# Performance work log

Measured on AMD Instinct MI355X. Metric: run time of the kernel, lower is better.

Reference implementation:

```python
import jax, jax.numpy as jnp
import numpy as np

D = 128
L_SIZE = 65536
C_SIZE = 32768
E = 262144
N_ITERS = 4


def _mlp(x, w1, b1, w2, b2):
    # 2-layer satbench MLP: Linear -> relu -> Linear
    return jax.nn.relu(x @ w1 + b1) @ w2 + b2


def setup_inputs() -> dict:
    key = jax.random.key(0)
    ks = iter(jax.random.split(key, 32))

    def lin(fi, fo):
        # torch nn.Linear default init, stored as (in, out)
        bound = 1.0 / np.sqrt(fi)
        w = jax.random.uniform(next(ks), (fi, fo), minval=-bound, maxval=bound, dtype=jnp.float32)
        b = jax.random.uniform(next(ks), (fo,), minval=-bound, maxval=bound, dtype=jnp.float32)
        return w, b

    s = np.sqrt(2.0 / D).astype(np.float32)
    inp = {}
    inp['l_edge_index'] = jax.random.randint(next(ks), (E,), 0, L_SIZE, dtype=jnp.int64)
    inp['c_edge_index'] = jax.random.randint(next(ks), (E,), 0, C_SIZE, dtype=jnp.int64)
    inp['l_init'] = jax.random.normal(next(ks), (1, D), dtype=jnp.float32) * s
    inp['c_init'] = jax.random.normal(next(ks), (1, D), dtype=jnp.float32) * s
    inp['w_l2c1'], inp['b_l2c1'] = lin(D, D)
    inp['w_l2c2'], inp['b_l2c2'] = lin(D, D)
    inp['w_c2l1'], inp['b_c2l1'] = lin(D, D)
    inp['w_c2l2'], inp['b_c2l2'] = lin(D, D)
    inp['w_l2l1'], inp['b_l2l1'] = lin(D, D)
    inp['w_l2l2'], inp['b_l2l2'] = lin(D, D)
    inp['w_cu'], inp['b_cu'] = lin(2 * D, D)
    inp['w_lu'], inp['b_lu'] = lin(3 * D, D)
    inp['l_size'] = L_SIZE
    inp['c_size'] = C_SIZE
    return inp


def reference(l_edge_index, c_edge_index, l_init, c_init,
              w_l2c1, b_l2c1, w_l2c2, b_l2c2,
              w_c2l1, b_c2l1, w_c2l2, b_c2l2,
              w_l2l1, b_l2l1, w_l2l2, b_l2l2,
              w_cu, b_cu, w_lu, b_lu, l_size, c_size):
    d = l_init.shape[1]
    ones = jnp.ones((l_edge_index.shape[0], 1), dtype=l_init.dtype)
    l_deg = jax.ops.segment_sum(ones, l_edge_index, num_segments=l_size)   # (L,1)
    c_deg = jax.ops.segment_sum(ones, c_edge_index, num_segments=c_size)   # (C,1)
    degree_norm = jnp.sqrt(l_deg[l_edge_index]) * jnp.sqrt(c_deg[c_edge_index])  # (E,1)

    l_emb = jnp.tile(l_init, (l_size, 1))  # (L,d)
    c_emb = jnp.tile(c_init, (c_size, 1))  # (C,d)

    def step(carry, _):
        l_emb, c_emb = carry
        l2c_msg = _mlp(l_emb, w_l2c1, b_l2c1, w_l2c2, b_l2c2)[l_edge_index]  # (E,d)
        c2l_msg = _mlp(c_emb, w_c2l1, b_c2l1, w_c2l2, b_c2l2)[c_edge_index]  # (E,d)
        # swap positive/negative literal partner embeddings (pairs are adjacent rows)
        l2l_in = l_emb.reshape(l_size // 2, 2, d)[:, ::-1, :].reshape(l_size, d)
        l2l_msg = _mlp(l2l_in, w_l2l1, b_l2l1, w_l2l2, b_l2l2)              # (L,d)
        l2c_aggr = jax.ops.segment_sum(l2c_msg / degree_norm, c_edge_index, num_segments=c_size)
        c_new = jnp.concatenate([c_emb, l2c_aggr], axis=1) @ w_cu + b_cu
        c2l_aggr = jax.ops.segment_sum(c2l_msg / degree_norm, l_edge_index, num_segments=l_size)
        l_new = jnp.concatenate([l_emb, c2l_aggr, l2l_msg], axis=1) @ w_lu + b_lu
        return (l_new, c_new), None

    (l_emb, c_emb), _ = jax.lax.scan(step, (l_emb, c_emb), None, length=N_ITERS)
    return l_emb
```

## Files before the change

kernel.cpp:

```cpp
#include <hip/hip_runtime.h>
#include <hip/hip_bf16.h>

#define D_ 128
#define L_ 65536
#define C_ 32768
#define E_ 262144

typedef __hip_bfloat16 bf16;
typedef __attribute__((ext_vector_type(8))) short short8;
typedef __attribute__((ext_vector_type(4))) float f32x4;

__global__ void detect_k(const unsigned short* __restrict__ wmem,
                         const int* __restrict__ li, int* __restrict__ flags) {
    int t = blockIdx.x * 512 + threadIdx.x;
    if (t < 8192) {
        unsigned short h = wmem[2 * t];
        float v = __bfloat162float(*(const bf16*)&h);
        if (!(fabsf(v) < 0.5f)) atomicOr(&flags[0], 1);
    }
    if (t < 2048) {
        if (li[2 * t + 1] != 0) atomicOr(&flags[1], 1);
    }
}

__device__ __forceinline__ void split2(float v, unsigned short& h, unsigned short& l) {
    bf16 bh = __float2bfloat16(v);
    float fh = __bfloat162float(bh);
    bf16 bl = __float2bfloat16(v - fh);
    h = *(unsigned short*)&bh;
    l = *(unsigned short*)&bl;
}

__device__ __forceinline__ float ldf(const void* s, int i, int isf32) {
    return isf32 ? ((const float*)s)[i] : __bfloat162float(((const bf16*)s)[i]);
}

__global__ void fixdeg_k(const int* __restrict__ ls, const int* __restrict__ cs,
                         int* __restrict__ ld_idx, int* __restrict__ cd_idx,
                         int* __restrict__ ldeg, int* __restrict__ cdeg,
                         const int* __restrict__ flags) {
    int i = blockIdx.x * 256 + threadIdx.x;
    int is32 = flags[1];
    if (i < E_) {
        int v = is32 ? ls[i] : ls[2 * i];
        v = min(max(v, 0), L_ - 1);
        ld_idx[i] = v;
        atomicAdd(&ldeg[v], 1);
    } else {
        int j = i - E_;
        int v = is32 ? cs[j] : cs[2 * j];
        v = min(max(v, 0), C_ - 1);
        cd_idx[j] = v;
        atomicAdd(&cdeg[v], 1);
    }
}

__global__ void cvtwb_k(const void* s0, const void* s1, const void* s2, const void* s3,
                        const void* s4, const void* s5, const void* s6, const void* s7,
                        const void* t0, const void* t1, const void* t2, const void* t3,
                        const void* t4, const void* t5, const void* t6, const void* t7,
                        unsigned short* __restrict__ hi, unsigned short* __restrict__ lo,
                        float* __restrict__ bb, const int* __restrict__ flags) {
    int i = blockIdx.x * 256 + threadIdx.x;
    int isf = flags[0];
    if (i >= 180224) {
        int j = i - 180224;
        const void* src;
        switch (j >> 7) {
            case 0: src = t0; break; case 1: src = t1; break;
            case 2: src = t2; break; case 3: src = t3; break;
            case 4: src = t4; break; case 5: src = t5; break;
            case 6: src = t6; break; default: src = t7; break;
        }
        bb[j] = ldf(src, j & 127, isf);
        return;
    }
    const void* src; int K, base;
    if      (i <  16384) { src = s0; K = 128; base = 0; }
    else if (i <  32768) { src = s1; K = 128; base = 16384; }
    else if (i <  49152) { src = s2; K = 128; base = 32768; }
    else if (i <  65536) { src = s3; K = 128; base = 49152; }
    else if (i <  81920) { src = s4; K = 128; base = 65536; }
    else if (i <  98304) { src = s5; K = 128; base = 81920; }
    else if (i < 131072) { src = s6; K = 256; base = 98304; }
    else                 { src = s7; K = 384; base = 131072; }
    int e = i - base;
    int k = e >> 7, n = e & 127;
    float v = ldf(src, e, isf);
    unsigned short h, l;
    split2(v, h, l);
    hi[base + n * K + k] = h;
    lo[base + n * K + k] = l;
}

__global__ void init2_k(const void* __restrict__ lv, const void* __restrict__ cv,
                        float* __restrict__ lemb, float* __restrict__ cemb,
                        const int* __restrict__ flags) {
    int i4 = blockIdx.x * 256 + threadIdx.x;
    int isf = flags[0];
    const void* src; float* dst; int o;
    if (i4 < L_ * 32) { src = lv; dst = lemb; o = i4; }
    else              { src = cv; dst = cemb; o = i4 - L_ * 32; }
    int j = (o & 31) * 4;
    float4 v;
    v.x = ldf(src, j + 0, isf);
    v.y = ldf(src, j + 1, isf);
    v.z = ldf(src, j + 2, isf);
    v.w = ldf(src, j + 3, isf);
    ((float4*)dst)[o] = v;
}

__global__ void scan1b_k(const int* __restrict__ ldeg, const int* __restrict__ cdeg,
                         int* __restrict__ lout, int* __restrict__ cout,
                         int* __restrict__ bsumL, int* __restrict__ bsumC) {
    __shared__ int s[256];
    const int* in; int* out; int* bs; int tile;
    if (blockIdx.x < 256) { in = ldeg; out = lout; bs = bsumL; tile = blockIdx.x; }
    else                  { in = cdeg; out = cout; bs = bsumC; tile = blockIdx.x - 256; }
    int i = tile * 256 + threadIdx.x;
    int v = in[i];
    s[threadIdx.x] = v;
    __syncthreads();
#pragma unroll
    for (int off = 1; off < 256; off <<= 1) {
        int t = (threadIdx.x >= off) ? s[threadIdx.x - off] : 0;
        __syncthreads();
        s[threadIdx.x] += t;
        __syncthreads();
    }
    out[i] = s[threadIdx.x] - v;
    if (threadIdx.x == 255) bs[tile] = s[255];
}

__global__ void scan2b_k(int* __restrict__ bL, int* __restrict__ bC) {
    __shared__ int s[256];
    int* b = blockIdx.x ? bC : bL;
    int nb = blockIdx.x ? 128 : 256;
    int v = (threadIdx.x < nb) ? b[threadIdx.x] : 0;
    s[threadIdx.x] = v;
    __syncthreads();
#pragma unroll
    for (int off = 1; off < 256; off <<= 1) {
        int t = (threadIdx.x >= off) ? s[threadIdx.x - off] : 0;
        __syncthreads();
        s[threadIdx.x] += t;
        __syncthreads();
    }
    if (threadIdx.x < nb) b[threadIdx.x] = s[threadIdx.x] - v;
}

__global__ void scan3b_k(int* __restrict__ lptr, int* __restrict__ cptr,
                         const int* __restrict__ bsumL, const int* __restrict__ bsumC,
                         int* __restrict__ lcur, int* __restrict__ ccur,
                         const int* __restrict__ ldeg, const int* __restrict__ cdeg,
                         float* __restrict__ invsq_l, float* __restrict__ invsq_c) {
    int b = blockIdx.x, t = threadIdx.x;
    if (b < 256) {
        int i = b * 256 + t;
        int v = lptr[i] + bsumL[b];
        lptr[i] = v; lcur[i] = v;
        int d = ldeg[i];
        invsq_l[i] = d ? rsqrtf((float)d) : 0.0f;
    } else {
        int i = (b - 256) * 256 + t;
        int v = cptr[i] + bsumC[b - 256];
        cptr[i] = v; ccur[i] = v;
        int d = cdeg[i];
        invsq_c[i] = d ? rsqrtf((float)d) : 0.0f;
    }
}

__global__ void place_k(const int* __restrict__ li, const int* __restrict__ ci,
                        int* __restrict__ lcur, int* __restrict__ ccur,
                        int* __restrict__ l_other, int* __restrict__ c_other) {
    int e = blockIdx.x * 256 + threadIdx.x;
    if (e >= E_) return;
    int l = li[e], c = ci[e];
    int p = atomicAdd(&ccur[c], 1);
    c_other[p] = l;
    int q = atomicAdd(&lcur[l], 1);
    l_other[q] = c;
}

__global__ __launch_bounds__(256) void gather2_k(
    const int* __restrict__ cptr, const int* __restrict__ cdeg, const int* __restrict__ c_other,
    const unsigned int* __restrict__ lmsg, const float* __restrict__ invsq_c, float* __restrict__ caggr,
    const int* __restrict__ lptr, const int* __restrict__ ldeg, const int* __restrict__ l_other,
    const unsigned int* __restrict__ cmsg, const float* __restrict__ invsq_l, float* __restrict__ laggr,
    int nC) {
    int node = (blockIdx.x * 256 + threadIdx.x) >> 6;
    int lane = threadIdx.x & 63;
    bool cside = node < nC;
    int j = cside ? node : node - nC;
    const int* ptr = cside ? cptr : lptr;
    const int* dg  = cside ? cdeg : ldeg;
    const int* oth = cside ? c_other : l_other;
    const unsigned int* msg = cside ? lmsg : cmsg;
    float sc = (cside ? invsq_c : invsq_l)[j];
    float* out = cside ? caggr : laggr;
    int s = ptr[j], cnt = dg[j];
    float2 a0 = {0.f, 0.f}, a1 = {0.f, 0.f};
    int k = 0;
    for (; k + 4 <= cnt; k += 4) {
        int o0 = oth[s + k], o1 = oth[s + k + 1], o2 = oth[s + k + 2], o3 = oth[s + k + 3];
        unsigned int u0 = msg[(size_t)o0 * 64 + lane];
        unsigned int u1 = msg[(size_t)o1 * 64 + lane];
        unsigned int u2 = msg[(size_t)o2 * 64 + lane];
        unsigned int u3 = msg[(size_t)o3 * 64 + lane];
        a0.x += __uint_as_float(u0 << 16) + __uint_as_float(u2 << 16);
        a0.y += __uint_as_float(u0 & 0xffff0000u) + __uint_as_float(u2 & 0xffff0000u);
        a1.x += __uint_as_float(u1 << 16) + __uint_as_float(u3 << 16);
        a1.y += __uint_as_float(u1 & 0xffff0000u) + __uint_as_float(u3 & 0xffff0000u);
    }
    for (; k < cnt; k++) {
        int o = oth[s + k];
        unsigned int u = msg[(size_t)o * 64 + lane];
        a0.x += __uint_as_float(u << 16);
        a0.y += __uint_as_float(u & 0xffff0000u);
    }
    a0.x = (a0.x + a1.x) * sc;
    a0.y = (a0.y + a1.y) * sc;
    *(float2*)&out[(size_t)j * D_ + 2 * lane] = a0;
}

__global__ __launch_bounds__(512, 4) void mlp3_k(
    const float* __restrict__ l_cur, const float* __restrict__ c_cur,
    const unsigned short* __restrict__ wt_hi, const unsigned short* __restrict__ wt_lo,
    const float* __restrict__ bb,
    const float* __restrict__ invsq_l, const float* __restrict__ invsq_c,
    bf16* __restrict__ l_msg, bf16* __restrict__ c_msg, bf16* __restrict__ l2lb,
    int nL, int nC) {
    __shared__ char smem[66048];
    unsigned short (*a_hi)[40] = (unsigned short(*)[40])(smem);
    unsigned short (*a_lo)[40] = (unsigned short(*)[40])(smem + 10240);
    unsigned short* h_hi = (unsigned short*)(smem);
    unsigned short* h_lo = (unsigned short*)(smem + 32768);
    float* scv = (float*)(smem + 65536);

    int b = blockIdx.x, seg, tile;
    if (b < nL)           { seg = 0; tile = b; }
    else if (b < nL + nC) { seg = 1; tile = b - nL; }
    else                  { seg = 2; tile = b - nL - nC; }
    const float* A = (seg == 1) ? c_cur : l_cur;
    bf16* outp = (seg == 0) ? l_msg : (seg == 1) ? c_msg : l2lb;
    const float* invsq = (seg == 0) ? invsq_l : (seg == 1) ? invsq_c : nullptr;
    const unsigned short* W1h = wt_hi + seg * 32768;
    const unsigned short* W1l = wt_lo + seg * 32768;
    const unsigned short* W2h = W1h + 16384;
    const unsigned short* W2l = W1l + 16384;
    const float* b1v = bb + seg * 256;
    const float* b2v = b1v + 128;
    const int swap = (seg == 2);

    const int t = threadIdx.x;
    const int br0 = tile * 128;
    const int w = t >> 6, lane = t & 63;
    const int wr = w >> 2, wc = w & 3;
    const int quad = lane >> 4, cl = lane & 15;

    if (t < 128) scv[t] = invsq ? invsq[br0 + t] : 1.0f;

    f32x4 acc[4][2];
#pragma unroll
    for (int i = 0; i < 4; i++)
#pragma unroll
        for (int j = 0; j < 2; j++) acc[i][j] = (f32x4){0.f, 0.f, 0.f, 0.f};

    for (int kt = 0; kt < 128; kt += 32) {
#pragma unroll
        for (int i = 0; i < 2; i++) {
            int f = t + 512 * i;
            int r = f >> 3, kq = f & 7;
            int gr = br0 + r;
            if (swap) gr ^= 1;
            const float4 v = *(const float4*)&A[(size_t)gr * D_ + kt + 4 * kq];
            unsigned short h0, l0, h1, l1, h2, l2, h3, l3;
            split2(v.x, h0, l0); split2(v.y, h1, l1);
            split2(v.z, h2, l2); split2(v.w, h3, l3);
            *(ushort4*)&a_hi[r][4 * kq] = make_ushort4(h0, h1, h2, h3);
            *(ushort4*)&a_lo[r][4 * kq] = make_ushort4(l0, l1, l2, l3);
        }
        __syncthreads();
        short8 af_h[4], af_l[4];
#pragma unroll
        for (int i = 0; i < 4; i++) {
            int row = 64 * wr + 16 * i + cl;
            af_h[i] = *(const short8*)&a_hi[row][quad * 8];
            af_l[i] = *(const short8*)&a_lo[row][quad * 8];
        }
#pragma unroll
        for (int j = 0; j < 2; j++) {
            int col = 32 * wc + 16 * j + cl;
            short8 bf_h = *(const short8*)&W1h[(size_t)col * 128 + kt + quad * 8];
            short8 bf_l = *(const short8*)&W1l[(size_t)col * 128 + kt + quad * 8];
#pragma unroll
            for (int i = 0; i < 4; i++) {
                acc[i][j] = __builtin_amdgcn_mfma_f32_16x16x32_bf16(af_h[i], bf_h, acc[i][j], 0, 0, 0);
                acc[i][j] = __builtin_amdgcn_mfma_f32_16x16x32_bf16(af_h[i], bf_l, acc[i][j], 0, 0, 0);
                acc[i][j] = __builtin_amdgcn_mfma_f32_16x16x32_bf16(af_l[i], bf_h, acc[i][j], 0, 0, 0);
            }
        }
        __syncthreads();
    }
#pragma unroll
    for (int j = 0; j < 2; j++) {
        int col = 32 * wc + 16 * j + cl;
        float bv = b1v[col];
        int g = col >> 3, go = col & 7;
#pragma unroll
        for (int i = 0; i < 4; i++) {
            int rloc = 64 * wr + 16 * i + quad * 4;
#pragma unroll
            for (int rg = 0; rg < 4; rg++) {
                float v = fmaxf(acc[i][j][rg] + bv, 0.0f);
                unsigned short hh, ll;
                split2(v, hh, ll);
                int r = rloc + rg;
                int off = r * 128 + ((g ^ (r & 15)) << 3) + go;
                h_hi[off] = hh;
                h_lo[off] = ll;
            }
        }
    }
    __syncthreads();
#pragma unroll
    for (int i = 0; i < 4; i++)
#pragma unroll
        for (int j = 0; j < 2; j++) acc[i][j] = (f32x4){0.f, 0.f, 0.f, 0.f};

    for (int kt = 0; kt < 128; kt += 32) {
        short8 af_h[4], af_l[4];
        int gbase = (kt >> 3) + quad;
#pragma unroll
        for (int i = 0; i < 4; i++) {
            int r = 64 * wr + 16 * i + cl;
            int off = r * 128 + ((gbase ^ cl) << 3);
            af_h[i] = *(const short8*)&h_hi[off];
            af_l[i] = *(const short8*)&h_lo[off];
        }
#pragma unroll
        for (int j = 0; j < 2; j++) {
            int col = 32 * wc + 16 * j + cl;
            const short8 bf_h = *(const short8*)&W2h[(size_t)col * 128 + kt + quad * 8];
            const short8 bf_l = *(const short8*)&W2l[(size_t)col * 128 + kt + quad * 8];
#pragma unroll
            for (int i = 0; i < 4; i++) {
                acc[i][j] = __builtin_amdgcn_mfma_f32_16x16x32_bf16(af_h[i], bf_h, acc[i][j], 0, 0, 0);
                acc[i][j] = __builtin_amdgcn_mfma_f32_16x16x32_bf16(af_h[i], bf_l, acc[i][j], 0, 0, 0);
                acc[i][j] = __builtin_amdgcn_mfma_f32_16x16x32_bf16(af_l[i], bf_h, acc[i][j], 0, 0, 0);
            }
        }
    }
#pragma unroll
    for (int j = 0; j < 2; j++) {
        int col = 32 * wc + 16 * j + cl;
        float bv = b2v[col];
#pragma unroll
        for (int i = 0; i < 4; i++) {
            int rloc = 64 * wr + 16 * i + quad * 4;
#pragma unroll
            for (int rg = 0; rg < 4; rg++)
                outp[(size_t)(br0 + rloc + rg) * D_ + col] =
                    __float2bfloat16((acc[i][j][rg] + bv) * scv[rloc + rg]);
        }
    }
}

template <int FINAL>
__global__ __launch_bounds__(256, 2) void update_k(
    const float* __restrict__ l_cur, const float* __restrict__ c_cur,
    const float* __restrict__ laggr, const float* __restrict__ caggr,
    const bf16* __restrict__ l2lb,
    const unsigned short* __restrict__ wt_hi, const unsigned short* __restrict__ wt_lo,
    const float* __restrict__ bb,
    float* __restrict__ c_nxt, float* __restrict__ l_nxt,
    void* __restrict__ dout, const int* __restrict__ flags) {
    __shared__ unsigned short a_hi[128][40], a_lo[128][40];
    __shared__ unsigned short b_hi[128][40], b_lo[128][40];
    const int t = threadIdx.x;
    int b = blockIdx.x;
    const bool cseg = (!FINAL) && (b < 256);
    const int tile = (FINAL || cseg) ? b : b - 256;
    const int K = cseg ? 256 : 384;
    const float* A0 = cseg ? c_cur : l_cur;
    const float* A1 = cseg ? caggr : laggr;
    const unsigned short* Wh = wt_hi + (cseg ? 98304 : 131072);
    const unsigned short* Wl = wt_lo + (cseg ? 98304 : 131072);
    const float* bias = bb + (cseg ? 768 : 896);
    const int br0 = tile * 128;
    const int w = t >> 6, lane = t & 63;
    const int wr = w >> 1, wc = w & 1;
    const int quad = lane >> 4, cl = lane & 15;

    f32x4 acc[4][4];
#pragma unroll
    for (int i = 0; i < 4; i++)
#pragma unroll
        for (int j = 0; j < 4; j++) acc[i][j] = (f32x4){0.f, 0.f, 0.f, 0.f};

    for (int kt = 0; kt < K; kt += 32) {
        const bool haslo = (kt < 256);
        const int koff = kt & 127;
#pragma unroll
        for (int i = 0; i < 4; i++) {
            int f = t + 256 * i;
            int r = f >> 3, kq = f & 7;
            if (haslo) {
                const float* As = (kt < 128) ? A0 : A1;
                const float4 v = *(const float4*)&As[(size_t)(br0 + r) * D_ + koff + 4 * kq];
                unsigned short h0, l0, h1, l1, h2, l2, h3, l3;
                split2(v.x, h0, l0); split2(v.y, h1, l1);
                split2(v.z, h2, l2); split2(v.w, h3, l3);
                *(ushort4*)&a_hi[r][4 * kq] = make_ushort4(h0, h1, h2, h3);
                *(ushort4*)&a_lo[r][4 * kq] = make_ushort4(l0, l1, l2, l3);
            } else {
                *(ushort4*)&a_hi[r][4 * kq] =
                    *(const ushort4*)&l2lb[(size_t)(br0 + r) * D_ + koff + 4 * kq];
            }
            *(ushort4*)&b_hi[r][4 * kq] = *(const ushort4*)&Wh[(size_t)r * K + kt + 4 * kq];
            *(ushort4*)&b_lo[r][4 * kq] = *(const ushort4*)&Wl[(size_t)r * K + kt + 4 * kq];
        }
        __syncthreads();
        short8 af_h[4], af_l[4];
#pragma unroll
        for (int i = 0; i < 4; i++) {
            int row = 64 * wr + 16 * i + cl;
            af_h[i] = *(const short8*)&a_hi[row][quad * 8];
            if (haslo) af_l[i] = *(const short8*)&a_lo[row][quad * 8];
        }
#pragma unroll
        for (int j = 0; j < 4; j++) {
            int col = 64 * wc + 16 * j + cl;
            short8 bf_h = *(const short8*)&b_hi[col][quad * 8];
            short8 bf_l = *(const short8*)&b_lo[col][quad * 8];
#pragma unroll
            for (int i = 0; i < 4; i++) {
                acc[i][j] = __builtin_amdgcn_mfma_f32_16x16x32_bf16(af_h[i], bf_h, acc[i][j], 0, 0, 0);
                acc[i][j] = __builtin_amdgcn_mfma_f32_16x16x32_bf16(af_h[i], bf_l, acc[i][j], 0, 0, 0);
                if (haslo)
                    acc[i][j] = __builtin_amdgcn_mfma_f32_16x16x32_bf16(af_l[i], bf_h, acc[i][j], 0, 0, 0);
            }
        }
        __syncthreads();
    }
    const int f32out = FINAL ? flags[0] : 1;
#pragma unroll
    for (int j = 0; j < 4; j++) {
        int col = 64 * wc + 16 * j + cl;
        float bv = bias[col];
#pragma unroll
        for (int i = 0; i < 4; i++) {
            int rbase = br0 + 64 * wr + 16 * i + quad * 4;
#pragma unroll
            for (int rg = 0; rg < 4; rg++) {
                float v = acc[i][j][rg] + bv;
                size_t idx = (size_t)(rbase + rg) * D_ + col;
                if (FINAL) {
                    if (f32out) ((float*)dout)[idx] = v;
                    else        ((bf16*)dout)[idx] = __float2bfloat16(v);
                } else {
                    (cseg ? c_nxt : l_nxt)[idx] = v;
                }
            }
        }
    }
}

extern "C" void kernel_launch(void* const* d_in, const int* in_sizes, int n_in,
                              void* d_out, int out_size, void* d_ws, size_t ws_size,
                              hipStream_t stream) {
    const int* li_raw = (const int*)d_in[0];
    const int* ci_raw = (const int*)d_in[1];

    float* ws = (float*)d_ws;
    float* lbuf0 = ws;
    float* lbuf1 = lbuf0 + (size_t)L_ * D_;
    float* l2lb  = lbuf1 + (size_t)L_ * D_;
    float* laggr = l2lb + (size_t)L_ * D_;
    float* cbuf0 = laggr + (size_t)L_ * D_;
    float* cbuf1 = cbuf0 + (size_t)C_ * D_;
    float* caggr = cbuf1 + (size_t)C_ * D_;
    float* invsq_l = caggr + (size_t)C_ * D_;
    float* invsq_c = invsq_l + L_;
    float* bb    = invsq_c + C_;
    unsigned short* wt_hi = (unsigned short*)(bb + 1024);
    unsigned short* wt_lo = wt_hi + 180224;
    int*   li    = (int*)(wt_lo + 180224);
    int*   ci    = li + E_;
    int*   l_other = ci + E_;
    int*   c_other = l_other + E_;
    int*   ldegi = c_other + E_;
    int*   cdegi = ldegi + L_;
    int*   lptr  = cdegi + C_;
    int*   cptr  = lptr + L_;
    int*   lcur  = cptr + C_;
    int*   ccur  = lcur + L_;
    int*   bsumL = ccur + C_;
    int*   bsumC = bsumL + 256;
    int*   flags = bsumC + 128;

    hipMemsetAsync(flags, 0, 2 * sizeof(int), stream);
    detect_k<<<16, 512, 0, stream>>>((const unsigned short*)d_in[4], li_raw, flags);

    hipMemsetAsync(ldegi, 0, (size_t)(L_ + C_) * sizeof(int), stream);
    fixdeg_k<<<2 * E_ / 256, 256, 0, stream>>>(li_raw, ci_raw, li, ci, ldegi, cdegi, flags);

    cvtwb_k<<<708, 256, 0, stream>>>(d_in[4], d_in[6], d_in[8], d_in[10], d_in[12],
                                     d_in[14], d_in[16], d_in[18],
                                     d_in[5], d_in[7], d_in[9], d_in[11], d_in[13],
                                     d_in[15], d_in[17], d_in[19], wt_hi, wt_lo, bb, flags);

    scan1b_k<<<384, 256, 0, stream>>>(ldegi, cdegi, lptr, cptr, bsumL, bsumC);
    scan2b_k<<<2, 256, 0, stream>>>(bsumL, bsumC);
    scan3b_k<<<384, 256, 0, stream>>>(lptr, cptr, bsumL, bsumC, lcur, ccur,
                                      ldegi, cdegi, invsq_l, invsq_c);
    place_k<<<E_ / 256, 256, 0, stream>>>(li, ci, lcur, ccur, l_other, c_other);

    init2_k<<<(L_ + C_) * 32 / 256, 256, 0, stream>>>(d_in[2], d_in[3], lbuf0, cbuf0, flags);

    float* l_cur = lbuf0; float* l_nxt = lbuf1;
    float* c_cur = cbuf0; float* c_nxt = cbuf1;

    const int nL = L_ / 128, nC = C_ / 128;
    for (int it = 0; it < 3; it++) {
        mlp3_k<<<2 * nL + nC, 512, 0, stream>>>(
            l_cur, c_cur, wt_hi, wt_lo, bb, invsq_l, invsq_c,
            (bf16*)l_nxt, (bf16*)c_nxt, (bf16*)l2lb, nL, nC);
        gather2_k<<<(C_ + L_) / 4, 256, 0, stream>>>(
            cptr, cdegi, c_other, (const unsigned int*)l_nxt, invsq_c, caggr,
            lptr, ldegi, l_other, (const unsigned int*)c_nxt, invsq_l, laggr, C_);
        update_k<0><<<768, 256, 0, stream>>>(
            l_cur, c_cur, laggr, caggr, (const bf16*)l2lb, wt_hi, wt_lo, bb,
            c_nxt, l_nxt, nullptr, flags);
        float* tmp = l_cur; l_cur = l_nxt; l_nxt = tmp;
        tmp = c_cur; c_cur = c_nxt; c_nxt = tmp;
    }
    mlp3_k<<<nC + nL, 512, 0, stream>>>(
        l_cur, c_cur, wt_hi, wt_lo, bb, invsq_l, invsq_c,
        (bf16*)l_nxt, (bf16*)c_nxt, (bf16*)l2lb, 0, nC);
    gather2_k<<<L_ / 4, 256, 0, stream>>>(
        cptr, cdegi, c_other, (const unsigned int*)l_nxt, invsq_c, caggr,
        lptr, ldegi, l_other, (const unsigned int*)c_nxt, invsq_l, laggr, 0);
    update_k<1><<<512, 256, 0, stream>>>(
        l_cur, c_cur, laggr, caggr, (const bf16*)l2lb, wt_hi, wt_lo, bb,
        nullptr, nullptr, d_out, flags);
}
```

Baseline: 696.2 us.

## Stage full A tile once in mlp3, double-buffer A and read weights from global in update

In the MLP kernel, the whole 128x128 input tile is loaded and split into hi/lo bf16 up front into larger LDS slices. This removes the per-k-step load and sync pairs and uses a 36-short row pitch read with two 8-byte loads. In the update kernel, A tiles are double-buffered with register prefetch of the next k-slice overlapping the MFMAs, and the B (weight) fragments are read straight from global/L2 instead of staged in LDS. The MLP kernel's LDS use grows, which may reduce occupancy, and the direct global weight reads may add latency.

```diff
diff --git a/kernel.cpp b/kernel.cpp
--- a/kernel.cpp
+++ b/kernel.cpp
@@ -8,7 +8,15 @@
 
 typedef __hip_bfloat16 bf16;
 typedef __attribute__((ext_vector_type(8))) short short8;
+typedef __attribute__((ext_vector_type(4))) short short4e;
 typedef __attribute__((ext_vector_type(4))) float f32x4;
+
+__device__ __forceinline__ short8 ld8lds(const unsigned short* p) {
+    union { short8 v; struct { short4e a, b; } s; } u;
+    u.s.a = *(const short4e*)p;
+    u.s.b = *(const short4e*)(p + 4);
+    return u.v;
+}
 
 __global__ void detect_k(const unsigned short* __restrict__ wmem,
                          const int* __restrict__ li, int* __restrict__ flags) {
@@ -230,12 +238,12 @@
     const float* __restrict__ invsq_l, const float* __restrict__ invsq_c,
     bf16* __restrict__ l_msg, bf16* __restrict__ c_msg, bf16* __restrict__ l2lb,
     int nL, int nC) {
-    __shared__ char smem[66048];
-    unsigned short (*a_hi)[40] = (unsigned short(*)[40])(smem);
-    unsigned short (*a_lo)[40] = (unsigned short(*)[40])(smem + 10240);
+    __shared__ char smem[74240];
+    unsigned short (*a_hi)[36] = (unsigned short(*)[36])(smem);
+    unsigned short (*a_lo)[36] = (unsigned short(*)[36])(smem + 36864);
     unsigned short* h_hi = (unsigned short*)(smem);
     unsigned short* h_lo = (unsigned short*)(smem + 32768);
-    float* scv = (float*)(smem + 65536);
+    float* scv = (float*)(smem + 73728);
 
     int b = blockIdx.x, seg, tile;
     if (b < nL)           { seg = 0; tile = b; }
@@ -266,27 +274,36 @@
 #pragma unroll
         for (int j = 0; j < 2; j++) acc[i][j] = (f32x4){0.f, 0.f, 0.f, 0.f};
 
+    float4 va[8];
+#pragma unroll
+    for (int i = 0; i < 8; i++) {
+        int f = t + 512 * i;
+        int r = f >> 5, kq = f & 31;
+        int gr = br0 + r;
+        if (swap) gr ^= 1;
+        va[i] = *(const float4*)&A[(size_t)gr * D_ + 4 * kq];
+    }
+#pragma unroll
+    for (int i = 0; i < 8; i++) {
+        int f = t + 512 * i;
+        int r = f >> 5, kq = f & 31;
+        int sl = kq >> 3, kc = kq & 7;
+        unsigned short h0, l0, h1, l1, h2, l2, h3, l3;
+        split2(va[i].x, h0, l0); split2(va[i].y, h1, l1);
+        split2(va[i].z, h2, l2); split2(va[i].w, h3, l3);
+        *(ushort4*)&a_hi[sl * 128 + r][4 * kc] = make_ushort4(h0, h1, h2, h3);
+        *(ushort4*)&a_lo[sl * 128 + r][4 * kc] = make_ushort4(l0, l1, l2, l3);
+    }
+    __syncthreads();
+
     for (int kt = 0; kt < 128; kt += 32) {
-#pragma unroll
-        for (int i = 0; i < 2; i++) {
-            int f = t + 512 * i;
-            int r = f >> 3, kq = f & 7;
-            int gr = br0 + r;
-            if (swap) gr ^= 1;
-            const float4 v = *(const float4*)&A[(size_t)gr * D_ + kt + 4 * kq];
-            unsigned short h0, l0, h1, l1, h2, l2, h3, l3;
-            split2(v.x, h0, l0); split2(v.y, h1, l1);
-            split2(v.z, h2, l2); split2(v.w, h3, l3);
-            *(ushort4*)&a_hi[r][4 * kq] = make_ushort4(h0, h1, h2, h3);
-            *(ushort4*)&a_lo[r][4 * kq] = make_ushort4(l0, l1, l2, l3);
-        }
-        __syncthreads();
+        const int sl = kt >> 5;
         short8 af_h[4], af_l[4];
 #pragma unroll
         for (int i = 0; i < 4; i++) {
-            int row = 64 * wr + 16 * i + cl;
-            af_h[i] = *(const short8*)&a_hi[row][quad * 8];
-            af_l[i] = *(const short8*)&a_lo[row][quad * 8];
+            int row = sl * 128 + 64 * wr + 16 * i + cl;
+            af_h[i] = ld8lds(&a_hi[row][quad * 8]);
+            af_l[i] = ld8lds(&a_lo[row][quad * 8]);
         }
 #pragma unroll
         for (int j = 0; j < 2; j++) {
@@ -300,8 +317,8 @@
                 acc[i][j] = __builtin_amdgcn_mfma_f32_16x16x32_bf16(af_l[i], bf_h, acc[i][j], 0, 0, 0);
             }
         }
-        __syncthreads();
-    }
+    }
+    __syncthreads();
 #pragma unroll
     for (int j = 0; j < 2; j++) {
         int col = 32 * wc + 16 * j + cl;
@@ -375,13 +392,13 @@
     const float* __restrict__ bb,
     float* __restrict__ c_nxt, float* __restrict__ l_nxt,
     void* __restrict__ dout, const int* __restrict__ flags) {
-    __shared__ unsigned short a_hi[128][40], a_lo[128][40];
-    __shared__ unsigned short b_hi[128][40], b_lo[128][40];
+    __shared__ unsigned short a_hi[2][128][40], a_lo[2][128][40];
     const int t = threadIdx.x;
     int b = blockIdx.x;
     const bool cseg = (!FINAL) && (b < 256);
     const int tile = (FINAL || cseg) ? b : b - 256;
     const int K = cseg ? 256 : 384;
+    const int NK = K >> 5;
     const float* A0 = cseg ? c_cur : l_cur;
     const float* A1 = cseg ? caggr : laggr;
     const unsigned short* Wh = wt_hi + (cseg ? 98304 : 131072);
@@ -391,6 +408,7 @@
     const int w = t >> 6, lane = t & 63;
     const int wr = w >> 1, wc = w & 1;
     const int quad = lane >> 4, cl = lane & 15;
+    const int sr = t >> 3, skq = t & 7;
 
     f32x4 acc[4][4];
 #pragma unroll
@@ -398,47 +416,75 @@
 #pragma unroll
         for (int j = 0; j < 4; j++) acc[i][j] = (f32x4){0.f, 0.f, 0.f, 0.f};
 
-    for (int kt = 0; kt < K; kt += 32) {
-        const bool haslo = (kt < 256);
-        const int koff = kt & 127;
-#pragma unroll
-        for (int i = 0; i < 4; i++) {
-            int f = t + 256 * i;
-            int r = f >> 3, kq = f & 7;
-            if (haslo) {
-                const float* As = (kt < 128) ? A0 : A1;
-                const float4 v = *(const float4*)&As[(size_t)(br0 + r) * D_ + koff + 4 * kq];
-                unsigned short h0, l0, h1, l1, h2, l2, h3, l3;
-                split2(v.x, h0, l0); split2(v.y, h1, l1);
-                split2(v.z, h2, l2); split2(v.w, h3, l3);
-                *(ushort4*)&a_hi[r][4 * kq] = make_ushort4(h0, h1, h2, h3);
-                *(ushort4*)&a_lo[r][4 * kq] = make_ushort4(l0, l1, l2, l3);
+    {
+        float4 v[4];
+#pragma unroll
+        for (int i = 0; i < 4; i++)
+            v[i] = *(const float4*)&A0[(size_t)(br0 + sr + 32 * i) * D_ + 4 * skq];
+#pragma unroll
+        for (int i = 0; i < 4; i++) {
+            unsigned short h0, l0, h1, l1, h2, l2, h3, l3;
+            split2(v[i].x, h0, l0); split2(v[i].y, h1, l1);
+            split2(v[i].z, h2, l2); split2(v[i].w, h3, l3);
+            *(ushort4*)&a_hi[0][sr + 32 * i][4 * skq] = make_ushort4(h0, h1, h2, h3);
+            *(ushort4*)&a_lo[0][sr + 32 * i][4 * skq] = make_ushort4(l0, l1, l2, l3);
+        }
+    }
+    __syncthreads();
+
+    for (int kt = 0; kt < NK; kt++) {
+        const int p = kt & 1;
+        const bool haslo = (kt < 8);
+        const bool hasnext = (kt + 1 < NK);
+        const bool nlo = (kt + 1 < 8);
+        float4 nv[4]; ushort4 nb[4];
+        if (hasnext) {
+            const int koff = ((kt + 1) * 32) & 127;
+            if (nlo) {
+                const float* As = (kt + 1 < 4) ? A0 : A1;
+#pragma unroll
+                for (int i = 0; i < 4; i++)
+                    nv[i] = *(const float4*)&As[(size_t)(br0 + sr + 32 * i) * D_ + koff + 4 * skq];
             } else {
-                *(ushort4*)&a_hi[r][4 * kq] =
-                    *(const ushort4*)&l2lb[(size_t)(br0 + r) * D_ + koff + 4 * kq];
-            }
-            *(ushort4*)&b_hi[r][4 * kq] = *(const ushort4*)&Wh[(size_t)r * K + kt + 4 * kq];
-            *(ushort4*)&b_lo[r][4 * kq] = *(const ushort4*)&Wl[(size_t)r * K + kt + 4 * kq];
-        }
-        __syncthreads();
+#pragma unroll
+                for (int i = 0; i < 4; i++)
+                    nb[i] = *(const ushort4*)&l2lb[(size_t)(br0 + sr + 32 * i) * D_ + koff + 4 * skq];
+            }
+        }
         short8 af_h[4], af_l[4];
 #pragma unroll
         for (int i = 0; i < 4; i++) {
             int row = 64 * wr + 16 * i + cl;
-            af_h[i] = *(const short8*)&a_hi[row][quad * 8];
-            if (haslo) af_l[i] = *(const short8*)&a_lo[row][quad * 8];
+            af_h[i] = *(const short8*)&a_hi[p][row][quad * 8];
+            if (haslo) af_l[i] = *(const short8*)&a_lo[p][row][quad * 8];
         }
 #pragma unroll
         for (int j = 0; j < 4; j++) {
             int col = 64 * wc + 16 * j + cl;
-            short8 bf_h = *(const short8*)&b_hi[col][quad * 8];
-            short8 bf_l = *(const short8*)&b_lo[col][quad * 8];
+            const short8 bf_h = *(const short8*)&Wh[(size_t)col * K + kt * 32 + quad * 8];
+            const short8 bf_l = *(const short8*)&Wl[(size_t)col * K + kt * 32 + quad * 8];
 #pragma unroll
             for (int i = 0; i < 4; i++) {
                 acc[i][j] = __builtin_amdgcn_mfma_f32_16x16x32_bf16(af_h[i], bf_h, acc[i][j], 0, 0, 0);
                 acc[i][j] = __builtin_amdgcn_mfma_f32_16x16x32_bf16(af_h[i], bf_l, acc[i][j], 0, 0, 0);
                 if (haslo)
                     acc[i][j] = __builtin_amdgcn_mfma_f32_16x16x32_bf16(af_l[i], bf_h, acc[i][j], 0, 0, 0);
+            }
+        }
+        if (hasnext) {
+            if (nlo) {
+#pragma unroll
+                for (int i = 0; i < 4; i++) {
+                    unsigned short h0, l0, h1, l1, h2, l2, h3, l3;
+                    split2(nv[i].x, h0, l0); split2(nv[i].y, h1, l1);
+                    split2(nv[i].z, h2, l2); split2(nv[i].w, h3, l3);
+                    *(ushort4*)&a_hi[p ^ 1][sr + 32 * i][4 * skq] = make_ushort4(h0, h1, h2, h3);
+                    *(ushort4*)&a_lo[p ^ 1][sr + 32 * i][4 * skq] = make_ushort4(l0, l1, l2, l3);
+                }
+            } else {
+#pragma unroll
+                for (int i = 0; i < 4; i++)
+                    *(ushort4*)&a_hi[p ^ 1][sr + 32 * i][4 * skq] = nb[i];
             }
         }
         __syncthreads();
```

Measured after the change: 762.0 us. 1.09x slower.

## Store embeddings and aggregates as pre-split bf16 hi/lo planes, double-buffer update tiles

Applied to the files above, without the earlier changes.

Embeddings and aggregation outputs are now stored as separate bf16 high/low planes instead of fp32. The split is done once, by the producer (init, gather, update epilogue), so mlp3 and update load ready-made MFMA operands without converting in their inner loops. update_k also drops its LDS staging of weights, reading B fragments straight from global memory. It gains a double-buffered A tile that prefetches the next K-slice into registers while MFMAs run. The catch is extra global traffic for weight reads, which rely on cache hits, and more register pressure from the prefetch.

```diff
diff --git a/kernel.cpp b/kernel.cpp
--- a/kernel.cpp
+++ b/kernel.cpp
@@ -94,20 +94,22 @@
 }
 
 __global__ void init2_k(const void* __restrict__ lv, const void* __restrict__ cv,
-                        float* __restrict__ lemb, float* __restrict__ cemb,
+                        unsigned short* __restrict__ lhi, unsigned short* __restrict__ llo,
+                        unsigned short* __restrict__ chi, unsigned short* __restrict__ clo,
                         const int* __restrict__ flags) {
     int i4 = blockIdx.x * 256 + threadIdx.x;
     int isf = flags[0];
-    const void* src; float* dst; int o;
-    if (i4 < L_ * 32) { src = lv; dst = lemb; o = i4; }
-    else              { src = cv; dst = cemb; o = i4 - L_ * 32; }
+    const void* src; unsigned short *dh, *dl; int o;
+    if (i4 < L_ * 32) { src = lv; dh = lhi; dl = llo; o = i4; }
+    else              { src = cv; dh = chi; dl = clo; o = i4 - L_ * 32; }
     int j = (o & 31) * 4;
-    float4 v;
-    v.x = ldf(src, j + 0, isf);
-    v.y = ldf(src, j + 1, isf);
-    v.z = ldf(src, j + 2, isf);
-    v.w = ldf(src, j + 3, isf);
-    ((float4*)dst)[o] = v;
+    ushort4 vh, vl;
+    split2(ldf(src, j + 0, isf), vh.x, vl.x);
+    split2(ldf(src, j + 1, isf), vh.y, vl.y);
+    split2(ldf(src, j + 2, isf), vh.z, vl.z);
+    split2(ldf(src, j + 3, isf), vh.w, vl.w);
+    *(ushort4*)&dh[(size_t)o * 4] = vh;
+    *(ushort4*)&dl[(size_t)o * 4] = vl;
 }
 
 __global__ void scan1b_k(const int* __restrict__ ldeg, const int* __restrict__ cdeg,
@@ -184,9 +186,11 @@
 
 __global__ __launch_bounds__(256) void gather2_k(
     const int* __restrict__ cptr, const int* __restrict__ cdeg, const int* __restrict__ c_other,
-    const unsigned int* __restrict__ lmsg, const float* __restrict__ invsq_c, float* __restrict__ caggr,
+    const unsigned int* __restrict__ lmsg, const float* __restrict__ invsq_c,
+    unsigned short* __restrict__ cag_hi, unsigned short* __restrict__ cag_lo,
     const int* __restrict__ lptr, const int* __restrict__ ldeg, const int* __restrict__ l_other,
-    const unsigned int* __restrict__ cmsg, const float* __restrict__ invsq_l, float* __restrict__ laggr,
+    const unsigned int* __restrict__ cmsg, const float* __restrict__ invsq_l,
+    unsigned short* __restrict__ lag_hi, unsigned short* __restrict__ lag_lo,
     int nC) {
     int node = (blockIdx.x * 256 + threadIdx.x) >> 6;
     int lane = threadIdx.x & 63;
@@ -197,7 +201,8 @@
     const int* oth = cside ? c_other : l_other;
     const unsigned int* msg = cside ? lmsg : cmsg;
     float sc = (cside ? invsq_c : invsq_l)[j];
-    float* out = cside ? caggr : laggr;
+    unsigned short* ohi = cside ? cag_hi : lag_hi;
+    unsigned short* olo = cside ? cag_lo : lag_lo;
     int s = ptr[j], cnt = dg[j];
     float2 a0 = {0.f, 0.f}, a1 = {0.f, 0.f};
     int k = 0;
@@ -220,11 +225,16 @@
     }
     a0.x = (a0.x + a1.x) * sc;
     a0.y = (a0.y + a1.y) * sc;
-    *(float2*)&out[(size_t)j * D_ + 2 * lane] = a0;
+    unsigned short h0, l0, h1, l1;
+    split2(a0.x, h0, l0);
+    split2(a0.y, h1, l1);
+    ((unsigned int*)ohi)[(size_t)j * 64 + lane] = (unsigned int)h0 | ((unsigned int)h1 << 16);
+    ((unsigned int*)olo)[(size_t)j * 64 + lane] = (unsigned int)l0 | ((unsigned int)l1 << 16);
 }
 
 __global__ __launch_bounds__(512, 4) void mlp3_k(
-    const float* __restrict__ l_cur, const float* __restrict__ c_cur,
+    const unsigned short* __restrict__ l_hi, const unsigned short* __restrict__ l_lo,
+    const unsigned short* __restrict__ c_hi, const unsigned short* __restrict__ c_lo,
     const unsigned short* __restrict__ wt_hi, const unsigned short* __restrict__ wt_lo,
     const float* __restrict__ bb,
     const float* __restrict__ invsq_l, const float* __restrict__ invsq_c,
@@ -241,7 +251,8 @@
     if (b < nL)           { seg = 0; tile = b; }
     else if (b < nL + nC) { seg = 1; tile = b - nL; }
     else                  { seg = 2; tile = b - nL - nC; }
-    const float* A = (seg == 1) ? c_cur : l_cur;
+    const unsigned short* Ah = (seg == 1) ? c_hi : l_hi;
+    const unsigned short* Al = (seg == 1) ? c_lo : l_lo;
     bf16* outp = (seg == 0) ? l_msg : (seg == 1) ? c_msg : l2lb;
     const float* invsq = (seg == 0) ? invsq_l : (seg == 1) ? invsq_c : nullptr;
     const unsigned short* W1h = wt_hi + seg * 32768;
@@ -269,16 +280,12 @@
     for (int kt = 0; kt < 128; kt += 32) {
 #pragma unroll
         for (int i = 0; i < 2; i++) {
-            int f = t + 512 * i;
-            int r = f >> 3, kq = f & 7;
+            int s = t + 512 * i;
+            int r = s >> 3, kq = s & 7;
             int gr = br0 + r;
             if (swap) gr ^= 1;
-            const float4 v = *(const float4*)&A[(size_t)gr * D_ + kt + 4 * kq];
-            unsigned short h0, l0, h1, l1, h2, l2, h3, l3;
-            split2(v.x, h0, l0); split2(v.y, h1, l1);
-            split2(v.z, h2, l2); split2(v.w, h3, l3);
-            *(ushort4*)&a_hi[r][4 * kq] = make_ushort4(h0, h1, h2, h3);
-            *(ushort4*)&a_lo[r][4 * kq] = make_ushort4(l0, l1, l2, l3);
+            *(ushort4*)&a_hi[r][4 * kq] = *(const ushort4*)&Ah[(size_t)gr * D_ + kt + 4 * kq];
+            *(ushort4*)&a_lo[r][4 * kq] = *(const ushort4*)&Al[(size_t)gr * D_ + kt + 4 * kq];
         }
         __syncthreads();
         short8 af_h[4], af_l[4];
@@ -368,22 +375,27 @@
 
 template <int FINAL>
 __global__ __launch_bounds__(256, 2) void update_k(
-    const float* __restrict__ l_cur, const float* __restrict__ c_cur,
-    const float* __restrict__ laggr, const float* __restrict__ caggr,
+    const unsigned short* __restrict__ l_hi, const unsigned short* __restrict__ l_lo,
+    const unsigned short* __restrict__ c_hi, const unsigned short* __restrict__ c_lo,
+    const unsigned short* __restrict__ lag_hi, const unsigned short* __restrict__ lag_lo,
+    const unsigned short* __restrict__ cag_hi, const unsigned short* __restrict__ cag_lo,
     const bf16* __restrict__ l2lb,
     const unsigned short* __restrict__ wt_hi, const unsigned short* __restrict__ wt_lo,
     const float* __restrict__ bb,
-    float* __restrict__ c_nxt, float* __restrict__ l_nxt,
+    unsigned short* __restrict__ c_hi_n, unsigned short* __restrict__ c_lo_n,
+    unsigned short* __restrict__ l_hi_n, unsigned short* __restrict__ l_lo_n,
     void* __restrict__ dout, const int* __restrict__ flags) {
-    __shared__ unsigned short a_hi[128][40], a_lo[128][40];
-    __shared__ unsigned short b_hi[128][40], b_lo[128][40];
+    __shared__ unsigned short a_hi[2][128][40], a_lo[2][128][40];
     const int t = threadIdx.x;
     int b = blockIdx.x;
     const bool cseg = (!FINAL) && (b < 256);
     const int tile = (FINAL || cseg) ? b : b - 256;
     const int K = cseg ? 256 : 384;
-    const float* A0 = cseg ? c_cur : l_cur;
-    const float* A1 = cseg ? caggr : laggr;
+    const int NK = K >> 5;
+    const unsigned short* A0h = cseg ? c_hi : l_hi;
+    const unsigned short* A0l = cseg ? c_lo : l_lo;
+    const unsigned short* AGh = cseg ? cag_hi : lag_hi;
+    const unsigned short* AGl = cseg ? cag_lo : lag_lo;
     const unsigned short* Wh = wt_hi + (cseg ? 98304 : 131072);
     const unsigned short* Wl = wt_lo + (cseg ? 98304 : 131072);
     const float* bias = bb + (cseg ? 768 : 896);
@@ -391,6 +403,7 @@
     const int w = t >> 6, lane = t & 63;
     const int wr = w >> 1, wc = w & 1;
     const int quad = lane >> 4, cl = lane & 15;
+    const int sr = t >> 3, skq = t & 7;
 
     f32x4 acc[4][4];
 #pragma unroll
@@ -398,41 +411,47 @@
 #pragma unroll
         for (int j = 0; j < 4; j++) acc[i][j] = (f32x4){0.f, 0.f, 0.f, 0.f};
 
-    for (int kt = 0; kt < K; kt += 32) {
-        const bool haslo = (kt < 256);
-        const int koff = kt & 127;
-#pragma unroll
-        for (int i = 0; i < 4; i++) {
-            int f = t + 256 * i;
-            int r = f >> 3, kq = f & 7;
-            if (haslo) {
-                const float* As = (kt < 128) ? A0 : A1;
-                const float4 v = *(const float4*)&As[(size_t)(br0 + r) * D_ + koff + 4 * kq];
-                unsigned short h0, l0, h1, l1, h2, l2, h3, l3;
-                split2(v.x, h0, l0); split2(v.y, h1, l1);
-                split2(v.z, h2, l2); split2(v.w, h3, l3);
-                *(ushort4*)&a_hi[r][4 * kq] = make_ushort4(h0, h1, h2, h3);
-                *(ushort4*)&a_lo[r][4 * kq] = make_ushort4(l0, l1, l2, l3);
-            } else {
-                *(ushort4*)&a_hi[r][4 * kq] =
-                    *(const ushort4*)&l2lb[(size_t)(br0 + r) * D_ + koff + 4 * kq];
-            }
-            *(ushort4*)&b_hi[r][4 * kq] = *(const ushort4*)&Wh[(size_t)r * K + kt + 4 * kq];
-            *(ushort4*)&b_lo[r][4 * kq] = *(const ushort4*)&Wl[(size_t)r * K + kt + 4 * kq];
-        }
-        __syncthreads();
+#pragma unroll
+    for (int i = 0; i < 4; i++) {
+        size_t go = (size_t)(br0 + sr + 32 * i) * D_ + 4 * skq;
+        *(ushort4*)&a_hi[0][sr + 32 * i][4 * skq] = *(const ushort4*)&A0h[go];
+        *(ushort4*)&a_lo[0][sr + 32 * i][4 * skq] = *(const ushort4*)&A0l[go];
+    }
+    __syncthreads();
+
+    for (int kt = 0; kt < NK; kt++) {
+        const int p = kt & 1;
+        const bool haslo = (kt < 8);
+        const bool hasnext = (kt + 1 < NK);
+        const bool nlo = (kt + 1 < 8);
+        ushort4 nh[4], nl[4];
+        if (hasnext) {
+            const int kn = kt + 1;
+            const unsigned short* sh;
+            const unsigned short* sl = nullptr;
+            int koff;
+            if (kn < 4)      { sh = A0h; sl = A0l; koff = kn * 32; }
+            else if (kn < 8) { sh = AGh; sl = AGl; koff = (kn - 4) * 32; }
+            else             { sh = (const unsigned short*)l2lb; koff = (kn - 8) * 32; }
+#pragma unroll
+            for (int i = 0; i < 4; i++) {
+                size_t go = (size_t)(br0 + sr + 32 * i) * D_ + koff + 4 * skq;
+                nh[i] = *(const ushort4*)&sh[go];
+                if (nlo) nl[i] = *(const ushort4*)&sl[go];
+            }
+        }
         short8 af_h[4], af_l[4];
 #pragma unroll
         for (int i = 0; i < 4; i++) {
             int row = 64 * wr + 16 * i + cl;
-            af_h[i] = *(const short8*)&a_hi[row][quad * 8];
-            if (haslo) af_l[i] = *(const short8*)&a_lo[row][quad * 8];
+            af_h[i] = *(const short8*)&a_hi[p][row][quad * 8];
+            if (haslo) af_l[i] = *(const short8*)&a_lo[p][row][quad * 8];
         }
 #pragma unroll
         for (int j = 0; j < 4; j++) {
             int col = 64 * wc + 16 * j + cl;
-            short8 bf_h = *(const short8*)&b_hi[col][quad * 8];
-            short8 bf_l = *(const short8*)&b_lo[col][quad * 8];
+            const short8 bf_h = *(const short8*)&Wh[(size_t)col * K + kt * 32 + quad * 8];
+            const short8 bf_l = *(const short8*)&Wl[(size_t)col * K + kt * 32 + quad * 8];
 #pragma unroll
             for (int i = 0; i < 4; i++) {
                 acc[i][j] = __builtin_amdgcn_mfma_f32_16x16x32_bf16(af_h[i], bf_h, acc[i][j], 0, 0, 0);
@@ -441,9 +460,18 @@
                     acc[i][j] = __builtin_amdgcn_mfma_f32_16x16x32_bf16(af_l[i], bf_h, acc[i][j], 0, 0, 0);
             }
         }
+        if (hasnext) {
+#pragma unroll
+            for (int i = 0; i < 4; i++) {
+                *(ushort4*)&a_hi[p ^ 1][sr + 32 * i][4 * skq] = nh[i];
+                if (nlo) *(ushort4*)&a_lo[p ^ 1][sr + 32 * i][4 * skq] = nl[i];
+            }
+        }
         __syncthreads();
     }
     const int f32out = FINAL ? flags[0] : 1;
+    unsigned short* Oh = cseg ? c_hi_n : l_hi_n;
+    unsigned short* Ol = cseg ? c_lo_n : l_lo_n;
 #pragma unroll
     for (int j = 0; j < 4; j++) {
         int col = 64 * wc + 16 * j + cl;
@@ -459,7 +487,10 @@
                     if (f32out) ((float*)dout)[idx] = v;
                     else        ((bf16*)dout)[idx] = __float2bfloat16(v);
                 } else {
-                    (cseg ? c_nxt : l_nxt)[idx] = v;
+                    unsigned short hh, ll;
+                    split2(v, hh, ll);
+                    Oh[idx] = hh;
+                    Ol[idx] = ll;
                 }
             }
         }
@@ -472,15 +503,19 @@
     const int* li_raw = (const int*)d_in[0];
     const int* ci_raw = (const int*)d_in[1];
 
-    float* ws = (float*)d_ws;
-    float* lbuf0 = ws;
-    float* lbuf1 = lbuf0 + (size_t)L_ * D_;
-    float* l2lb  = lbuf1 + (size_t)L_ * D_;
-    float* laggr = l2lb + (size_t)L_ * D_;
-    float* cbuf0 = laggr + (size_t)L_ * D_;
-    float* cbuf1 = cbuf0 + (size_t)C_ * D_;
-    float* caggr = cbuf1 + (size_t)C_ * D_;
-    float* invsq_l = caggr + (size_t)C_ * D_;
+    const size_t LD = (size_t)L_ * D_;
+    const size_t CD = (size_t)C_ * D_;
+    unsigned short* us = (unsigned short*)d_ws;
+    unsigned short* l_hi[2] = { us,          us + 2 * LD };
+    unsigned short* l_lo[2] = { us + LD,     us + 3 * LD };
+    unsigned short* c_hi[2] = { us + 4 * LD,          us + 4 * LD + 2 * CD };
+    unsigned short* c_lo[2] = { us + 4 * LD + CD,     us + 4 * LD + 3 * CD };
+    unsigned short* lag_hi = us + 4 * LD + 4 * CD;
+    unsigned short* lag_lo = lag_hi + LD;
+    unsigned short* cag_hi = lag_lo + LD;
+    unsigned short* cag_lo = cag_hi + CD;
+    bf16* l2lb_p = (bf16*)(cag_lo + CD);
+    float* invsq_l = (float*)((unsigned short*)l2lb_p + LD);
     float* invsq_c = invsq_l + L_;
     float* bb    = invsq_c + C_;
     unsigned short* wt_hi = (unsigned short*)(bb + 1024);
@@ -516,32 +551,36 @@
                                       ldegi, cdegi, invsq_l, invsq_c);
     place_k<<<E_ / 256, 256, 0, stream>>>(li, ci, lcur, ccur, l_other, c_other);
 
-    init2_k<<<(L_ + C_) * 32 / 256, 256, 0, stream>>>(d_in[2], d_in[3], lbuf0, cbuf0, flags);
-
-    float* l_cur = lbuf0; float* l_nxt = lbuf1;
-    float* c_cur = cbuf0; float* c_nxt = cbuf1;
+    init2_k<<<(L_ + C_) * 32 / 256, 256, 0, stream>>>(
+        d_in[2], d_in[3], l_hi[0], l_lo[0], c_hi[0], c_lo[0], flags);
 
     const int nL = L_ / 128, nC = C_ / 128;
+    int cur = 0;
     for (int it = 0; it < 3; it++) {
+        int nxt = cur ^ 1;
         mlp3_k<<<2 * nL + nC, 512, 0, stream>>>(
-            l_cur, c_cur, wt_hi, wt_lo, bb, invsq_l, invsq_c,
-            (bf16*)l_nxt, (bf16*)c_nxt, (bf16*)l2lb, nL, nC);
+            l_hi[cur], l_lo[cur], c_hi[cur], c_lo[cur], wt_hi, wt_lo, bb,
+            invsq_l, invsq_c,
+            (bf16*)l_lo[nxt], (bf16*)c_lo[nxt], l2lb_p, nL, nC);
         gather2_k<<<(C_ + L_) / 4, 256, 0, stream>>>(
-            cptr, cdegi, c_other, (const unsigned int*)l_nxt, invsq_c, caggr,
-            lptr, ldegi, l_other, (const unsigned int*)c_nxt, invsq_l, laggr, C_);
+            cptr, cdegi, c_other, (const unsigned int*)l_lo[nxt], invsq_c, cag_hi, cag_lo,
+            lptr, ldegi, l_other, (const unsigned int*)c_lo[nxt], invsq_l, lag_hi, lag_lo, C_);
         update_k<0><<<768, 256, 0, stream>>>(
-            l_cur, c_cur, laggr, caggr, (const bf16*)l2lb, wt_hi, wt_lo, bb,
-            c_nxt, l_nxt, nullptr, flags);
-        float* tmp = l_cur; l_cur = l_nxt; l_nxt = tmp;
-        tmp = c_cur; c_cur = c_nxt; c_nxt = tmp;
-    }
+            l_hi[cur], l_lo[cur], c_hi[cur], c_lo[cur],
+            lag_hi, lag_lo, cag_hi, cag_lo, l2lb_p, wt_hi, wt_lo, bb,
+            c_hi[nxt], c_lo[nxt], l_hi[nxt], l_lo[nxt], nullptr, flags);
+        cur = nxt;
+    }
+    int nxt = cur ^ 1;
     mlp3_k<<<nC + nL, 512, 0, stream>>>(
-        l_cur, c_cur, wt_hi, wt_lo, bb, invsq_l, invsq_c,
-        (bf16*)l_nxt, (bf16*)c_nxt, (bf16*)l2lb, 0, nC);
+        l_hi[cur], l_lo[cur], c_hi[cur], c_lo[cur], wt_hi, wt_lo, bb,
+        invsq_l, invsq_c,
+        (bf16*)l_lo[nxt], (bf16*)c_lo[nxt], l2lb_p, 0, nC);
     gather2_k<<<L_ / 4, 256, 0, stream>>>(
-        cptr, cdegi, c_other, (const unsigned int*)l_nxt, invsq_c, caggr,
-        lptr, ldegi, l_other, (const unsigned int*)c_nxt, invsq_l, laggr, 0);
+        cptr, cdegi, c_other, (const unsigned int*)l_lo[nxt], invsq_c, cag_hi, cag_lo,
+        lptr, ldegi, l_other, (const unsigned int*)c_lo[nxt], invsq_l, lag_hi, lag_lo, 0);
     update_k<1><<<512, 256, 0, stream>>>(
-        l_cur, c_cur, laggr, caggr, (const bf16*)l2lb, wt_hi, wt_lo, bb,
-        nullptr, nullptr, d_out, flags);
-}
+        l_hi[cur], l_lo[cur], c_hi[cur], c_lo[cur],
+        lag_hi, lag_lo, cag_hi, cag_lo, l2lb_p, wt_hi, wt_lo, bb,
+        nullptr, nullptr, nullptr, nullptr, d_out, flags);
+}
```

Result: slower. 732.5 us (+5.2%).
